# Optimization experiments

Measured on AMD Instinct MI355X. Metric: run time of the kernel, lower is better.

## Reference

```python
import jax, jax.numpy as jnp
import numpy as np

N = 50000
H = 4
C = 32  # hidden_channels // heads
NEG_SLOPE = 0.2


def gat_layer(x, W, a_src, a_dst, b, src, dst):
    # x: [N, F_in]; W: [F_in, H*C]; a_src/a_dst: [H, C]; b: [H*C]
    h = (x @ W).reshape(N, H, C)                      # [N, H, C]
    alpha_src = jnp.sum(h * a_src, axis=-1)           # [N, H]
    alpha_dst = jnp.sum(h * a_dst, axis=-1)           # [N, H]
    e = jax.nn.leaky_relu(alpha_src[src] + alpha_dst[dst], NEG_SLOPE)  # [E, H]
    # softmax over incoming edges per destination node (stable)
    m = jax.ops.segment_max(e, dst, num_segments=N)   # [N, H]
    p = jnp.exp(e - m[dst])                           # [E, H]
    s = jax.ops.segment_sum(p, dst, num_segments=N)   # [N, H]
    alpha = p / s[dst]                                # [E, H]
    msg = h[src] * alpha[:, :, None]                  # [E, H, C]
    out = jax.ops.segment_sum(msg, dst, num_segments=N)  # [N, H, C]
    return out.reshape(N, H * C) + b


def setup_inputs() -> dict:
    key = jax.random.key(0)
    ks = jax.random.split(key, 12)
    E = 1600000
    x = jax.random.normal(ks[0], (N, 128), dtype=jnp.float32)
    edge_index = jax.random.randint(ks[1], (2, E), 0, N, dtype=jnp.int32)
    s = 0.08
    return {
        "x": x,
        "edge_index": edge_index,
        "W1": jax.random.normal(ks[2], (128, H * C), dtype=jnp.float32) * s,
        "a_src1": jax.random.normal(ks[3], (H, C), dtype=jnp.float32) * s,
        "a_dst1": jax.random.normal(ks[4], (H, C), dtype=jnp.float32) * s,
        "b1": jnp.zeros((H * C,), dtype=jnp.float32),
        "W2": jax.random.normal(ks[5], (H * C, H * C), dtype=jnp.float32) * s,
        "a_src2": jax.random.normal(ks[6], (H, C), dtype=jnp.float32) * s,
        "a_dst2": jax.random.normal(ks[7], (H, C), dtype=jnp.float32) * s,
        "b2": jnp.zeros((H * C,), dtype=jnp.float32),
    }


def reference(x, edge_index, W1, a_src1, a_dst1, b1, W2, a_src2, a_dst2, b2):
    # PyG GATConv default add_self_loops=True: append (i -> i) edges
    loops = jnp.arange(N, dtype=edge_index.dtype)
    src = jnp.concatenate([edge_index[0], loops])
    dst = jnp.concatenate([edge_index[1], loops])
    # layer 1 + ELU (dropout is identity in eval mode)
    h = gat_layer(x, W1, a_src1, a_dst1, b1, src, dst)
    h = jax.nn.elu(h)
    # layer 2 + ELU
    h = gat_layer(h, W2, a_src2, a_dst2, b2, src, dst)
    h = jax.nn.elu(h)
    return h
```

## Files before the change

### kernel.cpp

```cpp
#include <hip/hip_runtime.h>
#include <hip/hip_bf16.h>

typedef _Float16 half8 __attribute__((ext_vector_type(8)));
typedef float f32x4 __attribute__((ext_vector_type(4)));

static __device__ __forceinline__ float bf2f_lo(unsigned u) {
    return __uint_as_float(u << 16);
}
static __device__ __forceinline__ float bf2f_hi(unsigned u) {
    return __uint_as_float(u & 0xffff0000u);
}
static __device__ __forceinline__ unsigned f2bf_rne_bits(float f) {
    unsigned u = __float_as_uint(f);
    return u + 0x7fffu + ((u >> 16) & 1u);
}
static __device__ __forceinline__ unsigned pack_bf2(float a, float b) {
    return (f2bf_rne_bits(a) >> 16) | (f2bf_rne_bits(b) & 0xffff0000u);
}
static __device__ __forceinline__ float pfun(float e) {
    e = fmaxf(e, 0.2f * e);
    return __expf(e);
}

#define CHUNK 4096

__global__ void kb_zero(int* bucketCount, int NBK) {
    int i = blockIdx.x * 256 + threadIdx.x;
    if (i < NBK) bucketCount[i] = 0;
}

__global__ void kb_count(const int* __restrict__ dst, int* bucketCount,
                         int E, int T, int NBK) {
    __shared__ int cnt[256];
    const int tid = threadIdx.x;
    const int beg = blockIdx.x * CHUNK;
    const int end = min(beg + CHUNK, T);
    cnt[tid] = 0;
    __syncthreads();
    for (int i = beg + tid; i < end; i += 256) {
        int d = (i < E) ? dst[i] : (i - E);
        atomicAdd(&cnt[d >> 8], 1);
    }
    __syncthreads();
    if (tid < NBK && cnt[tid] > 0) atomicAdd(&bucketCount[tid], cnt[tid]);
}

__global__ void kb_scan(const int* __restrict__ bucketCount, int* bucketBase,
                        int* bucketCursor, int* row_ptr, int NBK, int N, int total) {
    __shared__ int sm[256];
    const int tid = threadIdx.x;
    int v = (tid < NBK) ? bucketCount[tid] : 0;
    sm[tid] = v;
    __syncthreads();
    for (int off = 1; off < 256; off <<= 1) {
        int t = (tid >= off) ? sm[tid - off] : 0;
        __syncthreads();
        sm[tid] += t;
        __syncthreads();
    }
    if (tid < NBK) {
        int ex = sm[tid] - v;
        bucketBase[tid] = ex;
        bucketCursor[tid] = ex;
    }
    if (tid == 0) {
        bucketBase[NBK] = total;
        row_ptr[N] = total;
    }
}

__global__ void kb_place(const int* __restrict__ src, const int* __restrict__ dst,
                         int* bucketCursor, unsigned* __restrict__ barr,
                         int E, int T, int NBK) {
    __shared__ int cnt[256];
    __shared__ int wb[256];
    const int tid = threadIdx.x;
    const int beg = blockIdx.x * CHUNK;
    const int end = min(beg + CHUNK, T);
    cnt[tid] = 0;
    __syncthreads();
    for (int i = beg + tid; i < end; i += 256) {
        int d = (i < E) ? dst[i] : (i - E);
        atomicAdd(&cnt[d >> 8], 1);
    }
    __syncthreads();
    if (tid < NBK) {
        int c = cnt[tid];
        wb[tid] = (c > 0) ? atomicAdd(&bucketCursor[tid], c) : 0;
    }
    __syncthreads();
    cnt[tid] = 0;
    __syncthreads();
    for (int i = beg + tid; i < end; i += 256) {
        int s, d;
        if (i < E) { s = src[i]; d = dst[i]; }
        else       { s = i - E;  d = s; }
        int g = d >> 8;
        unsigned pk = (unsigned)s | ((unsigned)(d & 255) << 16);
        int r = atomicAdd(&cnt[g], 1);
        barr[wb[g] + r] = pk;
    }
}

__global__ void kb_csr(const unsigned* __restrict__ barr, const int* __restrict__ bucketBase,
                       int* __restrict__ row_ptr, int* __restrict__ col, int N) {
    __shared__ int cnt[256];
    __shared__ int sm[256];
    __shared__ int cur[256];
    const int tid = threadIdx.x;
    const int b = blockIdx.x;
    const int beg = bucketBase[b];
    const int end = bucketBase[b + 1];
    cnt[tid] = 0;
    __syncthreads();
    for (int i = beg + tid; i < end; i += 256)
        atomicAdd(&cnt[barr[i] >> 16], 1);
    __syncthreads();
    int v = cnt[tid];
    sm[tid] = v;
    __syncthreads();
    for (int off = 1; off < 256; off <<= 1) {
        int t = (tid >= off) ? sm[tid - off] : 0;
        __syncthreads();
        sm[tid] += t;
        __syncthreads();
    }
    int ex = sm[tid] - v;
    int n = b * 256 + tid;
    if (n < N) row_ptr[n] = beg + ex;
    cur[tid] = beg + ex;
    __syncthreads();
    for (int i = beg + tid; i < end; i += 256) {
        unsigned p = barr[i];
        int pos = atomicAdd(&cur[p >> 16], 1);
        col[pos] = (int)(p & 0xFFFFu);
    }
}

__launch_bounds__(256)
__global__ void k_gemm(const float* __restrict__ A, const float* __restrict__ W,
                       const float* __restrict__ a_src, const float* __restrict__ a_dst,
                       unsigned* __restrict__ Hout,
                       float* __restrict__ asrc_o, float* __restrict__ adst_o,
                       int nrows, int ntiles) {
    __shared__ _Float16 Wt[128 * 136];
    const int tid = threadIdx.x;
    for (int idx = tid; idx < 128 * 128 / 4; idx += 256) {
        int k = idx >> 5;
        int c4 = (idx & 31) * 4;
        float4 v = *(const float4*)&W[(size_t)k * 128 + c4];
        Wt[(c4 + 0) * 136 + k] = (_Float16)v.x;
        Wt[(c4 + 1) * 136 + k] = (_Float16)v.y;
        Wt[(c4 + 2) * 136 + k] = (_Float16)v.z;
        Wt[(c4 + 3) * 136 + k] = (_Float16)v.w;
    }
    __syncthreads();
    const int lane = tid & 63;
    const int m = lane & 15, quad = lane >> 4;

    half8 wf[4][8];
#pragma unroll
    for (int ks = 0; ks < 4; ++ks)
#pragma unroll
        for (int ct = 0; ct < 8; ++ct)
            wf[ks][ct] = *(half8*)&Wt[(ct * 16 + m) * 136 + ks * 32 + quad * 8];

    const int wv = (blockIdx.x * 256 + tid) >> 6;
    const int nwaves = gridDim.x * 4;
    for (int t = wv; t < ntiles; t += nwaves) {
        const int row = t * 16 + m;
        const int rc = min(row, nrows - 1);
        const float* ap = A + (size_t)rc * 128;
        f32x4 acc[8];
#pragma unroll
        for (int ct = 0; ct < 8; ++ct) acc[ct] = (f32x4){0.f, 0.f, 0.f, 0.f};
#pragma unroll
        for (int ks = 0; ks < 4; ++ks) {
            float4 x0 = *(const float4*)&ap[ks * 32 + quad * 8];
            float4 x1 = *(const float4*)&ap[ks * 32 + quad * 8 + 4];
            half8 af;
            af[0] = (_Float16)x0.x; af[1] = (_Float16)x0.y;
            af[2] = (_Float16)x0.z; af[3] = (_Float16)x0.w;
            af[4] = (_Float16)x1.x; af[5] = (_Float16)x1.y;
            af[6] = (_Float16)x1.z; af[7] = (_Float16)x1.w;
#pragma unroll
            for (int ct = 0; ct < 8; ++ct)
                acc[ct] = __builtin_amdgcn_mfma_f32_16x16x32_f16(wf[ks][ct], af, acc[ct], 0, 0, 0);
        }
        if (row < nrows) {
#pragma unroll
            for (int ct = 0; ct < 8; ++ct) {
                uint2 o;
                o.x = pack_bf2(acc[ct][0], acc[ct][1]);
                o.y = pack_bf2(acc[ct][2], acc[ct][3]);
                *(uint2*)&Hout[(size_t)row * 64 + ct * 8 + quad * 2] = o;
            }
        }
        float ps[4] = {0.f, 0.f, 0.f, 0.f}, pd[4] = {0.f, 0.f, 0.f, 0.f};
#pragma unroll
        for (int ct = 0; ct < 8; ++ct) {
            int hh = ct >> 1;
#pragma unroll
            for (int r = 0; r < 4; ++r) {
                int c = ct * 16 + quad * 4 + r;
                ps[hh] += acc[ct][r] * a_src[c];
                pd[hh] += acc[ct][r] * a_dst[c];
            }
        }
#pragma unroll
        for (int hh = 0; hh < 4; ++hh) {
            ps[hh] += __shfl_xor(ps[hh], 16); ps[hh] += __shfl_xor(ps[hh], 32);
            pd[hh] += __shfl_xor(pd[hh], 16); pd[hh] += __shfl_xor(pd[hh], 32);
        }
        if (row < nrows) {
            asrc_o[(size_t)row * 4 + quad] = ps[quad];
            adst_o[(size_t)row * 4 + quad] = pd[quad];
        }
    }
}

#define BAT 16
__launch_bounds__(256)
__global__ void k_aggr(const unsigned* __restrict__ h,
                       const float* __restrict__ asrc, const float* __restrict__ adst,
                       const float* __restrict__ bias,
                       const int* __restrict__ row_ptr, const int* __restrict__ col,
                       float* __restrict__ out, int N) {
    const int lane = threadIdx.x & 63;
    const int d = blockIdx.x * 4 + (threadIdx.x >> 6);
    if (d >= N) return;
    const int eb  = lane >> 2;
    const int hp  = lane & 3;
    const int hdc = lane >> 4;
    const float adv = adst[(size_t)d * 4 + hp];
    const int beg = row_ptr[d];
    const int end = row_ptr[d + 1];

    float ac0 = 0.f, ac1 = 0.f, sp = 0.f;
    int cv = 0;
    { int idx = beg + eb; if (idx < end) cv = col[idx]; }

    for (int j = beg; j < end; j += BAT) {
        int cvn = 0;
        { int idx = j + BAT + eb; if (idx < end) cvn = col[idx]; }

        float a = asrc[(size_t)(unsigned)cv * 4 + hp];
        float p = (j + eb < end) ? pfun(a + adv) : 0.f;
        sp += p;

        unsigned u[BAT];
#pragma unroll
        for (int k = 0; k < BAT; ++k) {
            int sk = __builtin_amdgcn_readlane(cv, 4 * k);
            u[k] = h[(size_t)(unsigned)sk * 64 + lane];
        }
#pragma unroll
        for (int k = 0; k < BAT; ++k) {
            float pk = __shfl(p, 4 * k + hdc);
            ac0 += pk * bf2f_lo(u[k]);
            ac1 += pk * bf2f_hi(u[k]);
        }
        cv = cvn;
    }

    sp += __shfl_xor(sp, 4);
    sp += __shfl_xor(sp, 8);
    sp += __shfl_xor(sp, 16);
    sp += __shfl_xor(sp, 32);
    float spv = __shfl(sp, hdc);
    float inv = 1.f / spv;

    int c = 2 * lane;
    float v0 = ac0 * inv + bias[c];
    float v1 = ac1 * inv + bias[c + 1];
    v0 = (v0 > 0.f) ? v0 : (__expf(v0) - 1.f);
    v1 = (v1 > 0.f) ? v1 : (__expf(v1) - 1.f);
    *(float2*)&out[(size_t)d * 128 + c] = make_float2(v0, v1);
}

extern "C" void kernel_launch(void* const* d_in, const int* in_sizes, int n_in,
                              void* d_out, int out_size, void* d_ws, size_t ws_size,
                              hipStream_t stream) {
    const float* x      = (const float*)d_in[0];
    const int*   ei     = (const int*)d_in[1];
    const float* W1     = (const float*)d_in[2];
    const float* a_src1 = (const float*)d_in[3];
    const float* a_dst1 = (const float*)d_in[4];
    const float* b1     = (const float*)d_in[5];
    const float* W2     = (const float*)d_in[6];
    const float* a_src2 = (const float*)d_in[7];
    const float* a_dst2 = (const float*)d_in[8];
    const float* b2     = (const float*)d_in[9];

    const int N = in_sizes[0] / 128;
    const int E = in_sizes[1] / 2;
    const int T = E + N;
    const int NBK = (N + 255) / 256;
    const int* src = ei;
    const int* dst = ei + E;

    char* w = (char*)d_ws;
    auto alloc = [&](size_t bytes) -> char* {
        char* p = w;
        w += (bytes + 255) & ~(size_t)255;
        return p;
    };
    unsigned* h_bf    = (unsigned*)alloc((size_t)N * 64 * 4);
    float*    o1      = (float*)alloc((size_t)N * 128 * 4);
    float*    asrc    = (float*)alloc((size_t)N * 4 * 4);
    float*    adst    = (float*)alloc((size_t)N * 4 * 4);
    int*      row_ptr = (int*)alloc((size_t)(N + 1) * 4);
    int*      col     = (int*)alloc((size_t)T * 4);
    int*      bCount  = (int*)alloc((size_t)NBK * 4);
    int*      bBase   = (int*)alloc((size_t)(NBK + 1) * 4);
    int*      bCursor = (int*)alloc((size_t)NBK * 4);
    unsigned* barr    = (unsigned*)o1;
    (void)ws_size; (void)n_in; (void)out_size;

    const int PB = (T + CHUNK - 1) / CHUNK;

    hipLaunchKernelGGL(kb_zero, dim3((NBK + 255) / 256), dim3(256), 0, stream, bCount, NBK);
    hipLaunchKernelGGL(kb_count, dim3(PB), dim3(256), 0, stream, dst, bCount, E, T, NBK);
    hipLaunchKernelGGL(kb_scan, dim3(1), dim3(256), 0, stream, bCount, bBase, bCursor, row_ptr, NBK, N, T);
    hipLaunchKernelGGL(kb_place, dim3(PB), dim3(256), 0, stream, src, dst, bCursor, barr, E, T, NBK);
    hipLaunchKernelGGL(kb_csr, dim3(NBK), dim3(256), 0, stream, barr, bBase, row_ptr, col, N);

    const int ntiles = (N + 15) / 16;
    const int GB = 512;
    const int AB = (N + 3) / 4;

    hipLaunchKernelGGL(k_gemm, dim3(GB), dim3(256), 0, stream, x, W1, a_src1, a_dst1, h_bf, asrc, adst, N, ntiles);
    hipLaunchKernelGGL(k_aggr, dim3(AB), dim3(256), 0, stream, h_bf, asrc, adst, b1, row_ptr, col, o1, N);
    hipLaunchKernelGGL(k_gemm, dim3(GB), dim3(256), 0, stream, o1, W2, a_src2, a_dst2, h_bf, asrc, adst, N, ntiles);
    hipLaunchKernelGGL(k_aggr, dim3(AB), dim3(256), 0, stream, h_bf, asrc, adst, b2, row_ptr, col, (float*)d_out, N);
}
```

Baseline: 306.7 us.

## Gather neighbor features with 16-byte loads and shuffled packed index/weight words

Rewrites the aggregation inner loop so each quarter-wave handles one edge. Each lane now issues one 16-byte load per edge instead of one 4-byte load, which cuts the number of gather instructions by four. The 16-bit source index and an fp16-rounded attention weight are packed into one word, so a single shuffle broadcasts both. The next batch's source attention scores are prefetched, and a cross-quarter shuffle reduction plus a remapped output column layout are added at the end. The trade-offs are fp16 rounding of the softmax weights and 16-bit node indices, which only hold while N stays below 65536.

```diff
diff --git a/kernel.cpp b/kernel.cpp
--- a/kernel.cpp
+++ b/kernel.cpp
@@ -1,8 +1,10 @@
 #include <hip/hip_runtime.h>
 #include <hip/hip_bf16.h>
+#include <hip/hip_fp16.h>
 
 typedef _Float16 half8 __attribute__((ext_vector_type(8)));
 typedef float f32x4 __attribute__((ext_vector_type(4)));
+typedef float f32x2 __attribute__((ext_vector_type(2)));
 
 static __device__ __forceinline__ float bf2f_lo(unsigned u) {
     return __uint_as_float(u << 16);
@@ -16,10 +18,6 @@
 }
 static __device__ __forceinline__ unsigned pack_bf2(float a, float b) {
     return (f2bf_rne_bits(a) >> 16) | (f2bf_rne_bits(b) & 0xffff0000u);
-}
-static __device__ __forceinline__ float pfun(float e) {
-    e = fmaxf(e, 0.2f * e);
-    return __expf(e);
 }
 
 #define CHUNK 4096
@@ -229,50 +227,84 @@
     const int lane = threadIdx.x & 63;
     const int d = blockIdx.x * 4 + (threadIdx.x >> 6);
     if (d >= N) return;
-    const int eb  = lane >> 2;
-    const int hp  = lane & 3;
-    const int hdc = lane >> 4;
+    const int eb = lane >> 2;
+    const int hp = lane & 3;
+    const int q  = lane >> 4;
+    const int sl = lane & 15;
+    const int hs = sl >> 2;
+    const int bidx = q * 4 + hs;
+
     const float adv = adst[(size_t)d * 4 + hp];
     const int beg = row_ptr[d];
     const int end = row_ptr[d + 1];
 
-    float ac0 = 0.f, ac1 = 0.f, sp = 0.f;
+    f32x2 acc[4];
+#pragma unroll
+    for (int i = 0; i < 4; ++i) acc[i] = (f32x2){0.f, 0.f};
+    float sp = 0.f;
+
     int cv = 0;
     { int idx = beg + eb; if (idx < end) cv = col[idx]; }
+    float av = asrc[(size_t)(unsigned)cv * 4 + hp];
 
     for (int j = beg; j < end; j += BAT) {
         int cvn = 0;
         { int idx = j + BAT + eb; if (idx < end) cvn = col[idx]; }
-
-        float a = asrc[(size_t)(unsigned)cv * 4 + hp];
-        float p = (j + eb < end) ? pfun(a + adv) : 0.f;
-        sp += p;
-
-        unsigned u[BAT];
-#pragma unroll
-        for (int k = 0; k < BAT; ++k) {
-            int sk = __builtin_amdgcn_readlane(cv, 4 * k);
-            u[k] = h[(size_t)(unsigned)sk * 64 + lane];
-        }
-#pragma unroll
-        for (int k = 0; k < BAT; ++k) {
-            float pk = __shfl(p, 4 * k + hdc);
-            ac0 += pk * bf2f_lo(u[k]);
-            ac1 += pk * bf2f_hi(u[k]);
-        }
-        cv = cvn;
-    }
-
+        float avn = asrc[(size_t)(unsigned)cvn * 4 + hp];
+
+        float e = av + adv;
+        e = fmaxf(e, 0.2f * e);
+        float p = (j + eb < end) ? __expf(e) : 0.f;
+        unsigned hb = (unsigned)__half_as_ushort(__float2half(p));
+        sp += __half2float(__ushort_as_half((unsigned short)hb));
+        unsigned w = (unsigned)(unsigned short)cv | (hb << 16);
+
+        unsigned wq[4];
+#pragma unroll
+        for (int k = 0; k < 4; ++k) wq[k] = (unsigned)__shfl((int)w, bidx + 16 * k);
+
+        uint4 u[4];
+#pragma unroll
+        for (int k = 0; k < 4; ++k) {
+            unsigned sv = wq[k] & 0xffffu;
+            u[k] = *(const uint4*)&h[(size_t)sv * 64 + sl * 4];
+        }
+#pragma unroll
+        for (int k = 0; k < 4; ++k) {
+            float pf = __half2float(__ushort_as_half((unsigned short)(wq[k] >> 16)));
+            f32x2 pv = {pf, pf};
+            f32x2 h0 = {bf2f_lo(u[k].x), bf2f_hi(u[k].x)};
+            f32x2 h1 = {bf2f_lo(u[k].y), bf2f_hi(u[k].y)};
+            f32x2 h2 = {bf2f_lo(u[k].z), bf2f_hi(u[k].z)};
+            f32x2 h3 = {bf2f_lo(u[k].w), bf2f_hi(u[k].w)};
+            acc[0] = __builtin_elementwise_fma(h0, pv, acc[0]);
+            acc[1] = __builtin_elementwise_fma(h1, pv, acc[1]);
+            acc[2] = __builtin_elementwise_fma(h2, pv, acc[2]);
+            acc[3] = __builtin_elementwise_fma(h3, pv, acc[3]);
+        }
+        cv = cvn; av = avn;
+    }
+
+#pragma unroll
+    for (int i = 0; i < 4; ++i) {
+#pragma unroll
+        for (int c = 0; c < 2; ++c) {
+            acc[i][c] += __shfl_xor(acc[i][c], 16);
+            acc[i][c] += __shfl_xor(acc[i][c], 32);
+        }
+    }
     sp += __shfl_xor(sp, 4);
     sp += __shfl_xor(sp, 8);
     sp += __shfl_xor(sp, 16);
     sp += __shfl_xor(sp, 32);
-    float spv = __shfl(sp, hdc);
-    float inv = 1.f / spv;
-
-    int c = 2 * lane;
-    float v0 = ac0 * inv + bias[c];
-    float v1 = ac1 * inv + bias[c + 1];
+    float s = __shfl(sp, hs);
+    float inv = 1.f / s;
+
+    float a0 = (q == 0) ? acc[0][0] : (q == 1) ? acc[1][0] : (q == 2) ? acc[2][0] : acc[3][0];
+    float a1 = (q == 0) ? acc[0][1] : (q == 1) ? acc[1][1] : (q == 2) ? acc[2][1] : acc[3][1];
+    int c = sl * 8 + q * 2;
+    float v0 = a0 * inv + bias[c];
+    float v1 = a1 * inv + bias[c + 1];
     v0 = (v0 > 0.f) ? v0 : (__expf(v0) - 1.f);
     v1 = (v1 > 0.f) ? v1 : (__expf(v1) - 1.f);
     *(float2*)&out[(size_t)d * 128 + c] = make_float2(v0, v1);
```

Result: no change. 307.4 us (+0.2%).

## Store features head-major and aggregate one head per block for cache locality

Applied to the files above, without the earlier changes.

The GEMM now writes the bf16 features and the attention scalars in a head-major layout ([head][node][...]). The aggregation kernel is restructured so each block handles a single head. Block indices interleave heads, so concurrently running blocks gather from a 1/4-size per-head feature slice that fits in cache more easily. Each wavefront now processes 4 destinations with 4 edges in flight per destination, using 16-byte gathers, software prefetch and shuffle reductions. The costs are extra redundant loads of col/row_ptr per head, possible load imbalance from padding to the max degree among grouped destinations, and more blocks overall.

```diff
diff --git a/kernel.cpp b/kernel.cpp
--- a/kernel.cpp
+++ b/kernel.cpp
@@ -1,8 +1,10 @@
 #include <hip/hip_runtime.h>
 #include <hip/hip_bf16.h>
+#include <hip/hip_fp16.h>
 
 typedef _Float16 half8 __attribute__((ext_vector_type(8)));
 typedef float f32x4 __attribute__((ext_vector_type(4)));
+typedef float f32x2 __attribute__((ext_vector_type(2)));
 
 static __device__ __forceinline__ float bf2f_lo(unsigned u) {
     return __uint_as_float(u << 16);
@@ -16,10 +18,6 @@
 }
 static __device__ __forceinline__ unsigned pack_bf2(float a, float b) {
     return (f2bf_rne_bits(a) >> 16) | (f2bf_rne_bits(b) & 0xffff0000u);
-}
-static __device__ __forceinline__ float pfun(float e) {
-    e = fmaxf(e, 0.2f * e);
-    return __expf(e);
 }
 
 #define CHUNK 4096
@@ -193,7 +191,7 @@
                 uint2 o;
                 o.x = pack_bf2(acc[ct][0], acc[ct][1]);
                 o.y = pack_bf2(acc[ct][2], acc[ct][3]);
-                *(uint2*)&Hout[(size_t)row * 64 + ct * 8 + quad * 2] = o;
+                *(uint2*)&Hout[((size_t)(ct >> 1) * nrows + row) * 16 + (ct & 1) * 8 + quad * 2] = o;
             }
         }
         float ps[4] = {0.f, 0.f, 0.f, 0.f}, pd[4] = {0.f, 0.f, 0.f, 0.f};
@@ -213,69 +211,102 @@
             pd[hh] += __shfl_xor(pd[hh], 16); pd[hh] += __shfl_xor(pd[hh], 32);
         }
         if (row < nrows) {
-            asrc_o[(size_t)row * 4 + quad] = ps[quad];
-            adst_o[(size_t)row * 4 + quad] = pd[quad];
-        }
-    }
-}
-
-#define BAT 16
+            asrc_o[(size_t)quad * nrows + row] = ps[quad];
+            adst_o[(size_t)quad * nrows + row] = pd[quad];
+        }
+    }
+}
+
 __launch_bounds__(256)
 __global__ void k_aggr(const unsigned* __restrict__ h,
-                       const float* __restrict__ asrc, const float* __restrict__ adst,
+                       const float* __restrict__ asrc,
+                       const float* __restrict__ adst,
                        const float* __restrict__ bias,
                        const int* __restrict__ row_ptr, const int* __restrict__ col,
-                       float* __restrict__ out, int N) {
+                       float* __restrict__ out, int N, int CPI) {
+    const int g8 = blockIdx.x & 7;
+    const int hh = g8 & 3;
+    const int inst = g8 >> 2;
+    const int chunk = blockIdx.x >> 3;
     const int lane = threadIdx.x & 63;
-    const int d = blockIdx.x * 4 + (threadIdx.x >> 6);
-    if (d >= N) return;
-    const int eb  = lane >> 2;
-    const int hp  = lane & 3;
-    const int hdc = lane >> 4;
-    const float adv = adst[(size_t)d * 4 + hp];
-    const int beg = row_ptr[d];
-    const int end = row_ptr[d + 1];
-
-    float ac0 = 0.f, ac1 = 0.f, sp = 0.f;
-    int cv = 0;
-    { int idx = beg + eb; if (idx < end) cv = col[idx]; }
-
-    for (int j = beg; j < end; j += BAT) {
-        int cvn = 0;
-        { int idx = j + BAT + eb; if (idx < end) cvn = col[idx]; }
-
-        float a = asrc[(size_t)(unsigned)cv * 4 + hp];
-        float p = (j + eb < end) ? pfun(a + adv) : 0.f;
+    const int dst_sub = lane >> 4;
+    const int eb2 = (lane >> 2) & 3;
+    const int q = lane & 3;
+
+    const int d = ((inst * CPI + chunk) * 4 + (threadIdx.x >> 6)) * 4 + dst_sub;
+    const int dc = min(d, N - 1);
+    const unsigned* __restrict__ hp = h + (size_t)hh * N * 16;
+    const float* __restrict__ as = asrc + (size_t)hh * N;
+    const float adv = adst[(size_t)hh * N + dc];
+    const int beg = row_ptr[dc];
+    const int end = row_ptr[dc + 1];
+
+    int its = (end - beg + 3) >> 2;
+    its = max(its, __shfl_xor(its, 16));
+    its = max(its, __shfl_xor(its, 32));
+
+    f32x2 acc[4];
+#pragma unroll
+    for (int i = 0; i < 4; ++i) acc[i] = (f32x2){0.f, 0.f};
+    float sp = 0.f;
+
+    int idx = beg + eb2;
+    int cv = col[min(idx, end - 1)];
+    float av = as[cv];
+    uint4 u = *(const uint4*)&hp[(size_t)(unsigned)cv * 16 + q * 4];
+
+    for (int it = 0; it < its - 1; ++it) {
+        int idx2 = idx + 4;
+        int cv2 = col[min(idx2, end - 1)];
+        float av2 = as[cv2];
+        uint4 u2 = *(const uint4*)&hp[(size_t)(unsigned)cv2 * 16 + q * 4];
+        float e = av + adv;
+        e = fmaxf(e, 0.2f * e);
+        float p = (idx < end) ? __expf(e) : 0.f;
         sp += p;
-
-        unsigned u[BAT];
-#pragma unroll
-        for (int k = 0; k < BAT; ++k) {
-            int sk = __builtin_amdgcn_readlane(cv, 4 * k);
-            u[k] = h[(size_t)(unsigned)sk * 64 + lane];
-        }
-#pragma unroll
-        for (int k = 0; k < BAT; ++k) {
-            float pk = __shfl(p, 4 * k + hdc);
-            ac0 += pk * bf2f_lo(u[k]);
-            ac1 += pk * bf2f_hi(u[k]);
-        }
-        cv = cvn;
-    }
-
-    sp += __shfl_xor(sp, 4);
-    sp += __shfl_xor(sp, 8);
-    sp += __shfl_xor(sp, 16);
-    sp += __shfl_xor(sp, 32);
-    float spv = __shfl(sp, hdc);
-    float inv = 1.f / spv;
-
-    int c = 2 * lane;
-    float v0 = ac0 * inv + bias[c];
-    float v1 = ac1 * inv + bias[c + 1];
-    v0 = (v0 > 0.f) ? v0 : (__expf(v0) - 1.f);
-    v1 = (v1 > 0.f) ? v1 : (__expf(v1) - 1.f);
-    *(float2*)&out[(size_t)d * 128 + c] = make_float2(v0, v1);
+        f32x2 pv = {p, p};
+        acc[0] = __builtin_elementwise_fma((f32x2){bf2f_lo(u.x), bf2f_hi(u.x)}, pv, acc[0]);
+        acc[1] = __builtin_elementwise_fma((f32x2){bf2f_lo(u.y), bf2f_hi(u.y)}, pv, acc[1]);
+        acc[2] = __builtin_elementwise_fma((f32x2){bf2f_lo(u.z), bf2f_hi(u.z)}, pv, acc[2]);
+        acc[3] = __builtin_elementwise_fma((f32x2){bf2f_lo(u.w), bf2f_hi(u.w)}, pv, acc[3]);
+        idx = idx2; cv = cv2; av = av2; u = u2;
+    }
+    {
+        float e = av + adv;
+        e = fmaxf(e, 0.2f * e);
+        float p = (idx < end) ? __expf(e) : 0.f;
+        sp += p;
+        f32x2 pv = {p, p};
+        acc[0] = __builtin_elementwise_fma((f32x2){bf2f_lo(u.x), bf2f_hi(u.x)}, pv, acc[0]);
+        acc[1] = __builtin_elementwise_fma((f32x2){bf2f_lo(u.y), bf2f_hi(u.y)}, pv, acc[1]);
+        acc[2] = __builtin_elementwise_fma((f32x2){bf2f_lo(u.z), bf2f_hi(u.z)}, pv, acc[2]);
+        acc[3] = __builtin_elementwise_fma((f32x2){bf2f_lo(u.w), bf2f_hi(u.w)}, pv, acc[3]);
+    }
+
+#pragma unroll
+    for (int off = 4; off <= 8; off <<= 1) {
+        sp += __shfl_xor(sp, off);
+#pragma unroll
+        for (int i = 0; i < 4; ++i) {
+            acc[i][0] += __shfl_xor(acc[i][0], off);
+            acc[i][1] += __shfl_xor(acc[i][1], off);
+        }
+    }
+
+    if (eb2 == 0 && d < N) {
+        float inv = 1.f / sp;
+        int cb = hh * 32 + q * 8;
+        float vv[8];
+#pragma unroll
+        for (int i = 0; i < 4; ++i) {
+            vv[2 * i]     = acc[i][0] * inv + bias[cb + 2 * i];
+            vv[2 * i + 1] = acc[i][1] * inv + bias[cb + 2 * i + 1];
+        }
+#pragma unroll
+        for (int i = 0; i < 8; ++i) vv[i] = (vv[i] > 0.f) ? vv[i] : (__expf(vv[i]) - 1.f);
+        *(float4*)&out[(size_t)d * 128 + cb]     = make_float4(vv[0], vv[1], vv[2], vv[3]);
+        *(float4*)&out[(size_t)d * 128 + cb + 4] = make_float4(vv[4], vv[5], vv[6], vv[7]);
+    }
 }
 
 extern "C" void kernel_launch(void* const* d_in, const int* in_sizes, int n_in,
@@ -327,10 +358,12 @@
 
     const int ntiles = (N + 15) / 16;
     const int GB = 512;
-    const int AB = (N + 3) / 4;
+    const int CPB = (N + 15) / 16;
+    const int CPI = (CPB + 1) / 2;
+    const int AB = 8 * CPI;
 
     hipLaunchKernelGGL(k_gemm, dim3(GB), dim3(256), 0, stream, x, W1, a_src1, a_dst1, h_bf, asrc, adst, N, ntiles);
-    hipLaunchKernelGGL(k_aggr, dim3(AB), dim3(256), 0, stream, h_bf, asrc, adst, b1, row_ptr, col, o1, N);
+    hipLaunchKernelGGL(k_aggr, dim3(AB), dim3(256), 0, stream, h_bf, asrc, adst, b1, row_ptr, col, o1, N, CPI);
     hipLaunchKernelGGL(k_gemm, dim3(GB), dim3(256), 0, stream, o1, W2, a_src2, a_dst2, h_bf, asrc, adst, N, ntiles);
-    hipLaunchKernelGGL(k_aggr, dim3(AB), dim3(256), 0, stream, h_bf, asrc, adst, b2, row_ptr, col, (float*)d_out, N);
-}
+    hipLaunchKernelGGL(k_aggr, dim3(AB), dim3(256), 0, stream, h_bf, asrc, adst, b2, row_ptr, col, (float*)d_out, N, CPI);
+}
```

Result: slower. 335.0 us (+9.2%).

## Merge CSR build and first GEMM into one launch; memset bucket counts

Applied to the files above, without the earlier changes.

Combines the per-bucket CSR construction and the layer-1 projection GEMM into a single kernel whose grid holds NBK CSR blocks followed by GB GEMM blocks. The two are independent, so they can run concurrently and one launch boundary goes away. The zero-fill kernel becomes hipMemsetAsync, and the aggregation inner loop uses explicit fmaf with the leaky-relu/exp inlined. The merged kernel has no __launch_bounds__ and shares one shared-memory buffer sized for the GEMM, so the CSR blocks reserve more LDS than they need, which may lower occupancy.

```diff
diff --git a/kernel.cpp b/kernel.cpp
--- a/kernel.cpp
+++ b/kernel.cpp
@@ -17,17 +17,8 @@
 static __device__ __forceinline__ unsigned pack_bf2(float a, float b) {
     return (f2bf_rne_bits(a) >> 16) | (f2bf_rne_bits(b) & 0xffff0000u);
 }
-static __device__ __forceinline__ float pfun(float e) {
-    e = fmaxf(e, 0.2f * e);
-    return __expf(e);
-}
 
 #define CHUNK 4096
-
-__global__ void kb_zero(int* bucketCount, int NBK) {
-    int i = blockIdx.x * 256 + threadIdx.x;
-    if (i < NBK) bucketCount[i] = 0;
-}
 
 __global__ void kb_count(const int* __restrict__ dst, int* bucketCount,
                          int E, int T, int NBK) {
@@ -102,48 +93,12 @@
     }
 }
 
-__global__ void kb_csr(const unsigned* __restrict__ barr, const int* __restrict__ bucketBase,
-                       int* __restrict__ row_ptr, int* __restrict__ col, int N) {
-    __shared__ int cnt[256];
-    __shared__ int sm[256];
-    __shared__ int cur[256];
-    const int tid = threadIdx.x;
-    const int b = blockIdx.x;
-    const int beg = bucketBase[b];
-    const int end = bucketBase[b + 1];
-    cnt[tid] = 0;
-    __syncthreads();
-    for (int i = beg + tid; i < end; i += 256)
-        atomicAdd(&cnt[barr[i] >> 16], 1);
-    __syncthreads();
-    int v = cnt[tid];
-    sm[tid] = v;
-    __syncthreads();
-    for (int off = 1; off < 256; off <<= 1) {
-        int t = (tid >= off) ? sm[tid - off] : 0;
-        __syncthreads();
-        sm[tid] += t;
-        __syncthreads();
-    }
-    int ex = sm[tid] - v;
-    int n = b * 256 + tid;
-    if (n < N) row_ptr[n] = beg + ex;
-    cur[tid] = beg + ex;
-    __syncthreads();
-    for (int i = beg + tid; i < end; i += 256) {
-        unsigned p = barr[i];
-        int pos = atomicAdd(&cur[p >> 16], 1);
-        col[pos] = (int)(p & 0xFFFFu);
-    }
-}
-
-__launch_bounds__(256)
-__global__ void k_gemm(const float* __restrict__ A, const float* __restrict__ W,
-                       const float* __restrict__ a_src, const float* __restrict__ a_dst,
-                       unsigned* __restrict__ Hout,
-                       float* __restrict__ asrc_o, float* __restrict__ adst_o,
-                       int nrows, int ntiles) {
-    __shared__ _Float16 Wt[128 * 136];
+static __device__ void gemm_body(_Float16* Wt , int bid, int GB,
+                                 const float* __restrict__ A, const float* __restrict__ W,
+                                 const float* __restrict__ a_src, const float* __restrict__ a_dst,
+                                 unsigned* __restrict__ Hout,
+                                 float* __restrict__ asrc_o, float* __restrict__ adst_o,
+                                 int nrows, int ntiles) {
     const int tid = threadIdx.x;
     for (int idx = tid; idx < 128 * 128 / 4; idx += 256) {
         int k = idx >> 5;
@@ -165,8 +120,8 @@
         for (int ct = 0; ct < 8; ++ct)
             wf[ks][ct] = *(half8*)&Wt[(ct * 16 + m) * 136 + ks * 32 + quad * 8];
 
-    const int wv = (blockIdx.x * 256 + tid) >> 6;
-    const int nwaves = gridDim.x * 4;
+    const int wv = (bid * 256 + tid) >> 6;
+    const int nwaves = GB * 4;
     for (int t = wv; t < ntiles; t += nwaves) {
         const int row = t * 16 + m;
         const int rc = min(row, nrows - 1);
@@ -217,6 +172,65 @@
             adst_o[(size_t)row * 4 + quad] = pd[quad];
         }
     }
+}
+
+__global__ void k_csr_gemm(const unsigned* __restrict__ barr, const int* __restrict__ bucketBase,
+                           int* __restrict__ row_ptr, int* __restrict__ col, int N, int NBK,
+                           const float* __restrict__ x, const float* __restrict__ W1,
+                           const float* __restrict__ a_src1, const float* __restrict__ a_dst1,
+                           unsigned* __restrict__ h_bf,
+                           float* __restrict__ asrc, float* __restrict__ adst,
+                           int ntiles, int GB) {
+    __shared__ __align__(16) char smem[128 * 136 * 2];
+    const int tid = threadIdx.x;
+    const int b = blockIdx.x;
+
+    if (b >= NBK) {
+        gemm_body((_Float16*)smem, b - NBK, GB, x, W1, a_src1, a_dst1,
+                  h_bf, asrc, adst, N, ntiles);
+        return;
+    }
+
+    int* cnt = (int*)smem;
+    int* sm  = (int*)smem + 256;
+    int* cur = (int*)smem + 512;
+    const int beg = bucketBase[b];
+    const int end = bucketBase[b + 1];
+    cnt[tid] = 0;
+    __syncthreads();
+    for (int i = beg + tid; i < end; i += 256)
+        atomicAdd(&cnt[barr[i] >> 16], 1);
+    __syncthreads();
+    int v = cnt[tid];
+    sm[tid] = v;
+    __syncthreads();
+    for (int off = 1; off < 256; off <<= 1) {
+        int t = (tid >= off) ? sm[tid - off] : 0;
+        __syncthreads();
+        sm[tid] += t;
+        __syncthreads();
+    }
+    int ex = sm[tid] - v;
+    int n = b * 256 + tid;
+    if (n < N) row_ptr[n] = beg + ex;
+    cur[tid] = beg + ex;
+    __syncthreads();
+    for (int i = beg + tid; i < end; i += 256) {
+        unsigned p = barr[i];
+        int pos = atomicAdd(&cur[p >> 16], 1);
+        col[pos] = (int)(p & 0xFFFFu);
+    }
+}
+
+__launch_bounds__(256)
+__global__ void k_gemm(const float* __restrict__ A, const float* __restrict__ W,
+                       const float* __restrict__ a_src, const float* __restrict__ a_dst,
+                       unsigned* __restrict__ Hout,
+                       float* __restrict__ asrc_o, float* __restrict__ adst_o,
+                       int nrows, int ntiles) {
+    __shared__ __align__(16) char smem[128 * 136 * 2];
+    gemm_body((_Float16*)smem, blockIdx.x, gridDim.x, A, W, a_src, a_dst,
+              Hout, asrc_o, adst_o, nrows, ntiles);
 }
 
 #define BAT 16
@@ -245,7 +259,9 @@
         { int idx = j + BAT + eb; if (idx < end) cvn = col[idx]; }
 
         float a = asrc[(size_t)(unsigned)cv * 4 + hp];
-        float p = (j + eb < end) ? pfun(a + adv) : 0.f;
+        float e = a + adv;
+        e = fmaxf(e, 0.2f * e);
+        float p = (j + eb < end) ? __expf(e) : 0.f;
         sp += p;
 
         unsigned u[BAT];
@@ -257,8 +273,8 @@
 #pragma unroll
         for (int k = 0; k < BAT; ++k) {
             float pk = __shfl(p, 4 * k + hdc);
-            ac0 += pk * bf2f_lo(u[k]);
-            ac1 += pk * bf2f_hi(u[k]);
+            ac0 = fmaf(pk, bf2f_lo(u[k]), ac0);
+            ac1 = fmaf(pk, bf2f_hi(u[k]), ac1);
         }
         cv = cvn;
     }
@@ -318,18 +334,17 @@
     (void)ws_size; (void)n_in; (void)out_size;
 
     const int PB = (T + CHUNK - 1) / CHUNK;
-
-    hipLaunchKernelGGL(kb_zero, dim3((NBK + 255) / 256), dim3(256), 0, stream, bCount, NBK);
+    const int ntiles = (N + 15) / 16;
+    const int GB = 512;
+    const int AB = (N + 3) / 4;
+
+    hipMemsetAsync(bCount, 0, (size_t)NBK * 4, stream);
     hipLaunchKernelGGL(kb_count, dim3(PB), dim3(256), 0, stream, dst, bCount, E, T, NBK);
     hipLaunchKernelGGL(kb_scan, dim3(1), dim3(256), 0, stream, bCount, bBase, bCursor, row_ptr, NBK, N, T);
     hipLaunchKernelGGL(kb_place, dim3(PB), dim3(256), 0, stream, src, dst, bCursor, barr, E, T, NBK);
-    hipLaunchKernelGGL(kb_csr, dim3(NBK), dim3(256), 0, stream, barr, bBase, row_ptr, col, N);
-
-    const int ntiles = (N + 15) / 16;
-    const int GB = 512;
-    const int AB = (N + 3) / 4;
-
-    hipLaunchKernelGGL(k_gemm, dim3(GB), dim3(256), 0, stream, x, W1, a_src1, a_dst1, h_bf, asrc, adst, N, ntiles);
+    hipLaunchKernelGGL(k_csr_gemm, dim3(NBK + GB), dim3(256), 0, stream,
+                       barr, bBase, row_ptr, col, N, NBK,
+                       x, W1, a_src1, a_dst1, h_bf, asrc, adst, ntiles, GB);
     hipLaunchKernelGGL(k_aggr, dim3(AB), dim3(256), 0, stream, h_bf, asrc, adst, b1, row_ptr, col, o1, N);
     hipLaunchKernelGGL(k_gemm, dim3(GB), dim3(256), 0, stream, o1, W2, a_src2, a_dst2, h_bf, asrc, adst, N, ntiles);
     hipLaunchKernelGGL(k_aggr, dim3(AB), dim3(256), 0, stream, h_bf, asrc, adst, b2, row_ptr, col, (float*)d_out, N);
```

Measured after the change: 385.5 us. +25.7%, slower.
